# Optimization experiments

Measured on AMD Instinct MI355X. Metric: run time of the kernel, lower is better.

## Reference

```python
import jax, jax.numpy as jnp
import numpy as np

C_S = 1024
H = 16
M = 1  # num_vector_messages
B, S = 2, 1024
SQRT3 = 3.0 ** 0.5
LN_EPS = 1e-5


def setup_inputs() -> dict:
    key = jax.random.key(0)
    ks = jax.random.split(key, 8)
    s = jax.random.normal(ks[0], (B, S, C_S), dtype=jnp.float32)
    # random proper-ish frames: orthonormalize random 3x3 via QR
    A = jax.random.normal(ks[1], (B, S, 3, 3), dtype=jnp.float32)
    rot, _ = jnp.linalg.qr(A)
    trans = jax.random.normal(ks[2], (B, S, 3), dtype=jnp.float32)
    affine_mask = jnp.ones((B, S), dtype=bool)
    sequence_id = jax.random.randint(ks[3], (B, S), 0, 4, dtype=jnp.int32)
    chain_id = jax.random.randint(ks[4], (B, S), 0, 4, dtype=jnp.int32)
    dim_proj = 4 * H * 3 + H * 3 * M
    ln_w = jnp.ones((C_S,), dtype=jnp.float32)
    w_proj = jax.random.normal(ks[5], (dim_proj, C_S), dtype=jnp.float32) / np.sqrt(C_S)
    w_out = jax.random.normal(ks[6], (C_S, H * 3 * M), dtype=jnp.float32) / np.sqrt(H * 3 * M)
    dist_scale = jnp.zeros((H,), dtype=jnp.float32)
    rot_scale = jnp.zeros((H,), dtype=jnp.float32)
    return {"s": s, "rot": rot, "trans": trans, "ln_w": ln_w, "w_proj": w_proj,
            "w_out": w_out, "dist_scale": dist_scale, "rot_scale": rot_scale,
            "affine_mask": affine_mask, "sequence_id": sequence_id, "chain_id": chain_id}


def reference(s, rot, trans, ln_w, w_proj, w_out, dist_scale, rot_scale,
              affine_mask, sequence_id, chain_id):
    b, n, c = s.shape
    h, m = H, M
    NEG = jnp.finfo(s.dtype).min
    # attention bias: 1.0 for same-sequence pairs, -inf for invalid frames / cross-chain
    seq_eq = (sequence_id[:, :, None] == sequence_id[:, None, :]).astype(s.dtype)
    bias = seq_eq[:, None]  # [b,1,s,s]
    bias = jnp.where(affine_mask[:, None, None, :], bias, NEG)
    chain_diff = chain_id[:, :, None] != chain_id[:, None, :]
    bias = jnp.where(chain_diff[:, None], NEG, bias)
    # LayerNorm (no bias)
    mu = jnp.mean(s, axis=-1, keepdims=True)
    var = jnp.var(s, axis=-1, keepdims=True)
    ns = (s - mu) / jnp.sqrt(var + LN_EPS) * ln_w
    p = jnp.einsum('bsc,dc->bsd', ns, w_proj)
    n_rot = h * 2 * 3 + h * 3 * m
    vec_rot = p[..., :n_rot].reshape(b, n, 2 * h + h * m, 3)
    vec_dist = p[..., n_rot:].reshape(b, n, 2 * h, 3)
    # rotate into global frame; dist vectors also translated
    rot_vecs = jnp.einsum('bsij,bshj->bshi', rot, vec_rot)
    q_rot, k_rot, value = rot_vecs[:, :, :h], rot_vecs[:, :, h:2 * h], rot_vecs[:, :, 2 * h:]
    dist_vecs = jnp.einsum('bsij,bshj->bshi', rot, vec_dist) + trans[:, :, None, :]
    q_dist, k_dist = dist_vecs[:, :, :h], dist_vecs[:, :, h:]
    # distance term [b,h,q,k]
    qd = q_dist.transpose(0, 2, 1, 3)  # b h s 3
    kd = k_dist.transpose(0, 2, 1, 3)
    diff = qd[:, :, :, None, :] - kd[:, :, None, :, :]
    distance_term = jnp.sqrt(jnp.sum(diff * diff, axis=-1)) / SQRT3
    rotation_term = jnp.einsum('bqhd,bkhd->bhqk', q_rot, k_rot) / SQRT3
    dw = jax.nn.softplus(dist_scale)[None, :, None, None]
    rw = jax.nn.softplus(rot_scale)[None, :, None, None]
    attn = rotation_term * rw - distance_term * dw + bias
    attn = jax.nn.softmax(attn, axis=-1)
    # value: b s (h m) 3 -> b h s (m 3)
    v = value.reshape(b, n, h, m, 3).transpose(0, 2, 1, 3, 4).reshape(b, h, n, m * 3)
    out = jnp.einsum('bhqk,bhkd->bhqd', attn, v)
    out = out.reshape(b, h, n, m, 3).transpose(0, 2, 1, 3, 4).reshape(b, n, h * m, 3)
    out = jnp.einsum('bsji,bshj->bshi', rot, out)  # inverse rotation R^T
    out = out.reshape(b, n, h * m * 3)
    out = jnp.where(affine_mask[..., None], out, 0.0)
    return jnp.einsum('bsd,cd->bsc', out, w_out)
```

## Files before the change

### kernel.cpp

```cpp
#include <hip/hip_runtime.h>
#include <math.h>

#define NB 2
#define NS 1024
#define NC 1024
#define NH 16
#define DIMP 240
#define KSPLIT 16
#define AKH 16

constexpr float INV_SQRT3 = 0.57735026919f;

__global__ __launch_bounds__(256) void pre_kernel(const float* __restrict__ s,
                                                  const float* __restrict__ lnw,
                                                  float* __restrict__ ns,
                                                  const float* __restrict__ wp,
                                                  float* __restrict__ wt) {
    __shared__ float sh[64 * 61];
    int tid = threadIdx.x;
    if (blockIdx.x < NB * NS) {
        int row = blockIdx.x;
        const float4* sp = (const float4*)(s + (size_t)row * NC);
        float4 v = sp[tid];
        float sum = v.x + v.y + v.z + v.w;
        float sq  = v.x*v.x + v.y*v.y + v.z*v.z + v.w*v.w;
        #pragma unroll
        for (int off = 32; off; off >>= 1) {
            sum += __shfl_down(sum, off);
            sq  += __shfl_down(sq, off);
        }
        float* s1 = sh; float* s2 = sh + 4;
        int wave = tid >> 6;
        if ((tid & 63) == 0) { s1[wave] = sum; s2[wave] = sq; }
        __syncthreads();
        float tot   = s1[0] + s1[1] + s1[2] + s1[3];
        float totsq = s2[0] + s2[1] + s2[2] + s2[3];
        float mu  = tot * (1.0f / NC);
        float var = totsq * (1.0f / NC) - mu * mu;
        float rstd = rsqrtf(var + 1e-5f);
        float4 w = ((const float4*)lnw)[tid];
        float4 o;
        o.x = (v.x - mu) * rstd * w.x;
        o.y = (v.y - mu) * rstd * w.y;
        o.z = (v.z - mu) * rstd * w.z;
        o.w = (v.w - mu) * rstd * w.w;
        ((float4*)(ns + (size_t)row * NC))[tid] = o;
    } else {
        int bx = blockIdx.x - NB * NS;
        int k0 = (bx & 15) * 64;
        int d0 = (bx >> 4) * 60;
        float (*T)[61] = (float (*)[61])sh;
        #pragma unroll
        for (int i = 0; i < 15; i++) {
            int idx = i * 256 + tid;
            int dd = idx >> 6, kk = idx & 63;
            T[kk][dd] = wp[(size_t)(d0 + dd) * NC + k0 + kk];
        }
        __syncthreads();
        #pragma unroll
        for (int i = 0; i < 15; i++) {
            int idx = i * 256 + tid;
            int kk = idx / 60, dd = idx % 60;
            wt[(size_t)(k0 + kk) * DIMP + d0 + dd] = T[kk][dd];
        }
    }
}

__global__ __launch_bounds__(256) void proj_kernel(const float* __restrict__ ns,
                                                   const float* __restrict__ wt,
                                                   float* __restrict__ pp,
                                                   int use_atomic) {
    int tid = threadIdx.x;
    int wave = tid >> 6, lane = tid & 63;
    int row0 = blockIdx.x * 32;
    int ky = blockIdx.y;
    int k0 = ky * 64;

    __shared__ float A[32][64];
    #pragma unroll
    for (int i = 0; i < 2; i++) {
        int idx = tid + i * 256;
        int r = idx >> 4, c4 = idx & 15;
        *(float4*)&A[r][c4 * 4] = *(const float4*)(ns + (size_t)(row0 + r) * NC + k0 + c4 * 4);
    }
    __syncthreads();

    int wr0 = wave * 8;
    int c0 = lane * 4;
    bool active = c0 < DIMP;
    int c0m = active ? c0 : (DIMP - 4);
    const float* wb = wt + (size_t)k0 * DIMP + c0m;

    float acc[8][4];
    #pragma unroll
    for (int r = 0; r < 8; r++)
        #pragma unroll
        for (int c = 0; c < 4; c++) acc[r][c] = 0.0f;

    float4 wa[4], wx[4];
    #pragma unroll
    for (int j = 0; j < 4; j++) wa[j] = *(const float4*)(wb + (size_t)j * DIMP);

    for (int g = 0; g < 16; g += 2) {
        #pragma unroll
        for (int j = 0; j < 4; j++)
            wx[j] = *(const float4*)(wb + (size_t)((g + 1) * 4 + j) * DIMP);
        #pragma unroll
        for (int r = 0; r < 8; r++) {
            float4 a4 = *(const float4*)&A[wr0 + r][g * 4];
            #pragma unroll
            for (int c = 0; c < 4; c++) {
                float* ac = &acc[r][c];
                *ac = fmaf(a4.x, ((const float*)&wa[0])[c], *ac);
                *ac = fmaf(a4.y, ((const float*)&wa[1])[c], *ac);
                *ac = fmaf(a4.z, ((const float*)&wa[2])[c], *ac);
                *ac = fmaf(a4.w, ((const float*)&wa[3])[c], *ac);
            }
        }
        int kn2 = (g + 2 < 16) ? (g + 2) * 4 : 0;
        #pragma unroll
        for (int j = 0; j < 4; j++)
            wa[j] = *(const float4*)(wb + (size_t)(kn2 + j) * DIMP);
        #pragma unroll
        for (int r = 0; r < 8; r++) {
            float4 a4 = *(const float4*)&A[wr0 + r][(g + 1) * 4];
            #pragma unroll
            for (int c = 0; c < 4; c++) {
                float* ac = &acc[r][c];
                *ac = fmaf(a4.x, ((const float*)&wx[0])[c], *ac);
                *ac = fmaf(a4.y, ((const float*)&wx[1])[c], *ac);
                *ac = fmaf(a4.z, ((const float*)&wx[2])[c], *ac);
                *ac = fmaf(a4.w, ((const float*)&wx[3])[c], *ac);
            }
        }
    }
    if (active) {
        if (use_atomic) {
            #pragma unroll
            for (int r = 0; r < 8; r++)
                #pragma unroll
                for (int c = 0; c < 4; c++)
                    atomicAdd(&pp[(size_t)(row0 + wr0 + r) * DIMP + c0 + c], acc[r][c]);
        } else {
            float* dst = pp + (size_t)ky * (NB * NS * DIMP);
            #pragma unroll
            for (int r = 0; r < 8; r++)
                *(float4*)(dst + (size_t)(row0 + wr0 + r) * DIMP + c0) =
                    make_float4(acc[r][0], acc[r][1], acc[r][2], acc[r][3]);
        }
    }
}

__global__ __launch_bounds__(256) void build_kernel(const float* __restrict__ pp, int nred,
                                                    const float* __restrict__ rot,
                                                    const float* __restrict__ trans,
                                                    const float* __restrict__ dist_scale,
                                                    const float* __restrict__ rot_scale,
                                                    const int* __restrict__ seq,
                                                    const int* __restrict__ chain,
                                                    const int* __restrict__ amask,
                                                    float4* __restrict__ qrb,
                                                    float4* __restrict__ qdb,
                                                    float4* __restrict__ kp) {
    int gid = blockIdx.x * 256 + threadIdx.x;
    if (gid >= NB * NS * 80) return;
    int j  = gid % 80;
    int bs = gid / 80;
    int b  = bs >> 10;
    int si = bs & 1023;
    int off = (j < 48) ? 3 * j : 144 + 3 * (j - 48);
    float vx = 0.0f, vy = 0.0f, vz = 0.0f;
    for (int ky = 0; ky < nred; ky++) {
        const float* pr = pp + (size_t)ky * (NB * NS * DIMP) + (size_t)bs * DIMP + off;
        vx += pr[0]; vy += pr[1]; vz += pr[2];
    }
    const float* R = rot + (size_t)bs * 9;
    float ox = R[0] * vx + R[1] * vy + R[2] * vz;
    float oy = R[3] * vx + R[4] * vy + R[5] * vz;
    float oz = R[6] * vx + R[7] * vy + R[8] * vz;
    if (j >= 48) {
        ox += trans[(size_t)bs * 3 + 0];
        oy += trans[(size_t)bs * 3 + 1];
        oz += trans[(size_t)bs * 3 + 2];
    }
    if (j < 16) {
        float sc = log1pf(__expf(rot_scale[j])) * INV_SQRT3;
        qrb[(size_t)(b * NH + j) * NS + si] = make_float4(ox * sc, oy * sc, oz * sc, 0.0f);
    } else if (j < 32) {
        int h = j - 16;
        float ck = (float)chain[bs] + 1000.0f * (float)(1 - amask[bs]);
        kp[((size_t)(b * NH + h) * NS + si) * 3 + 0] = make_float4(ox, oy, oz, ck);
    } else if (j < 48) {
        int h = j - 32;
        kp[((size_t)(b * NH + h) * NS + si) * 3 + 2] = make_float4(ox, oy, oz, 0.0f);
    } else if (j < 64) {
        int h = j - 48;
        float sc = log1pf(__expf(dist_scale[h])) * INV_SQRT3;
        qdb[(size_t)(b * NH + h) * NS + si] = make_float4(ox * sc, oy * sc, oz * sc, 0.0f);
    } else {
        int h = j - 64;
        float sc = log1pf(__expf(dist_scale[h])) * INV_SQRT3;
        kp[((size_t)(b * NH + h) * NS + si) * 3 + 1] =
            make_float4(ox * sc, oy * sc, oz * sc, (float)seq[bs]);
    }
}

__global__ __launch_bounds__(256) void attn_kernel(
    const float4* __restrict__ qrb, const float4* __restrict__ qdb,
    const float4* __restrict__ kp,
    float4* __restrict__ pacc) {
    __shared__ float4 kS[192];
    int bx = blockIdx.x;
    int ks = bx & (AKH - 1), qc = (bx >> 4) & 3, bh = bx >> 6;
    int tid = threadIdx.x;
    int q = qc * 256 + tid;
    int base = bh * NS;
    const float4* kb = kp + (size_t)base * 3;

    if (tid < 192) kS[tid] = kb[(size_t)ks * 192 + tid];
    __syncthreads();

    float4 a = qrb[base + q];
    float4 d = qdb[base + q];
    float cq = kb[(size_t)q * 3 + 0].w;
    float sq = kb[(size_t)q * 3 + 1].w;

    float l = 0.0f, ax = 0.0f, ay = 0.0f, az = 0.0f;
    #pragma unroll 4
    for (int j = 0; j < 64; j++) {
        float4 f0 = kS[j * 3 + 0];
        float4 f1 = kS[j * 3 + 1];
        float4 f2 = kS[j * 3 + 2];
        float rt = fmaf(a.x, f0.x, fmaf(a.y, f0.y, a.z * f0.z));
        float dx = d.x - f1.x, dy = d.y - f1.y, dz = d.z - f1.z;
        float dist = sqrtf(fmaf(dx, dx, fmaf(dy, dy, dz * dz)));
        float dc = f0.w - cq;
        float arg = fmaf(-100.0f, fabsf(dc), rt - dist) +
                    ((f1.w == sq) ? -15.0f : -16.0f);
        float pw = __expf(arg);
        l += pw;
        ax = fmaf(pw, f2.x, ax);
        ay = fmaf(pw, f2.y, ay);
        az = fmaf(pw, f2.z, az);
    }
    pacc[(size_t)ks * (32 * NS) + base + q] = make_float4(ax, ay, az, l);
}

__global__ __launch_bounds__(256) void attnfin_kernel(const float4* __restrict__ pacc,
                                                      const float4* __restrict__ kp,
                                                      const float* __restrict__ rot,
                                                      float* __restrict__ small) {
    int i = blockIdx.x * 256 + threadIdx.x;
    int bh = i >> 10, q = i & 1023;
    int b = bh >> 4, h = bh & 15;
    float4 s = make_float4(0.0f, 0.0f, 0.0f, 0.0f);
    #pragma unroll
    for (int j = 0; j < AKH; j++) {
        float4 t = pacc[(size_t)j * (32 * NS) + i];
        s.x += t.x; s.y += t.y; s.z += t.z; s.w += t.w;
    }
    float inv = 1.0f / s.w;
    float ox = s.x * inv, oy = s.y * inv, oz = s.z * inv;
    const float* R = rot + (size_t)(b * NS + q) * 9;
    float wx = R[0] * ox + R[3] * oy + R[6] * oz;
    float wy = R[1] * ox + R[4] * oy + R[7] * oz;
    float wz = R[2] * ox + R[5] * oy + R[8] * oz;
    float cq = kp[((size_t)bh * NS + q) * 3 + 0].w;
    if (cq >= 500.0f) { wx = 0; wy = 0; wz = 0; }
    float* o = small + (size_t)(b * NS + q) * 48 + h * 3;
    o[0] = wx; o[1] = wy; o[2] = wz;
}

__global__ __launch_bounds__(256) void outgemm_kernel(const float* __restrict__ small,
                                                      const float* __restrict__ wout,
                                                      float* __restrict__ out) {
    int c  = blockIdx.y * 256 + threadIdx.x;
    int r0 = blockIdx.x * 16;
    __shared__ float sm[16][48];
    for (int i = threadIdx.x; i < 16 * 48; i += 256)
        sm[i / 48][i % 48] = small[(size_t)(r0 + i / 48) * 48 + i % 48];
    __syncthreads();
    float w[48];
    #pragma unroll
    for (int d = 0; d < 48; d += 4) {
        float4 t = *(const float4*)(wout + (size_t)c * 48 + d);
        w[d] = t.x; w[d + 1] = t.y; w[d + 2] = t.z; w[d + 3] = t.w;
    }
    #pragma unroll 4
    for (int r = 0; r < 16; r++) {
        float acc = 0.0f;
        #pragma unroll
        for (int d = 0; d < 48; d++) acc = fmaf(w[d], sm[r][d], acc);
        out[(size_t)(r0 + r) * NC + c] = acc;
    }
}

extern "C" void kernel_launch(void* const* d_in, const int* in_sizes, int n_in,
                              void* d_out, int out_size, void* d_ws, size_t ws_size,
                              hipStream_t stream) {
    const float* s     = (const float*)d_in[0];
    const float* rot   = (const float*)d_in[1];
    const float* trans = (const float*)d_in[2];
    const float* lnw   = (const float*)d_in[3];
    const float* wproj = (const float*)d_in[4];
    const float* wout  = (const float*)d_in[5];
    const float* dsc   = (const float*)d_in[6];
    const float* rsc   = (const float*)d_in[7];
    const int* amask   = (const int*)d_in[8];
    const int* seq     = (const int*)d_in[9];
    const int* chain   = (const int*)d_in[10];
    float* out = (float*)d_out;

    float* ns = (float*)d_ws;
    float4* qrb = (float4*)(ns + (size_t)NB * NS * NC);
    float4* qdb = qrb + (size_t)NB * NH * NS;
    float4* kpk = qdb + (size_t)NB * NH * NS;
    float* small = (float*)(kpk + (size_t)3 * NB * NH * NS);
    float* pp = small + (size_t)NB * NS * 48;
    float* wt = (float*)qrb;
    float4* pacc = (float4*)pp;

    size_t need = ((char*)(pp + (size_t)KSPLIT * NB * NS * DIMP)) - (char*)d_ws;
    int use_atomic = (ws_size < need) ? 1 : 0;

    pre_kernel<<<NB * NS + 64, 256, 0, stream>>>(s, lnw, ns, wproj, wt);
    if (use_atomic) {
        hipMemsetAsync(pp, 0, (size_t)NB * NS * DIMP * sizeof(float), stream);
        proj_kernel<<<dim3(64, KSPLIT), 256, 0, stream>>>(ns, wt, pp, 1);
        build_kernel<<<(NB * NS * 80 + 255) / 256, 256, 0, stream>>>(pp, 1, rot, trans, dsc, rsc,
                                                                     seq, chain, amask, qrb, qdb, kpk);
    } else {
        proj_kernel<<<dim3(64, KSPLIT), 256, 0, stream>>>(ns, wt, pp, 0);
        build_kernel<<<(NB * NS * 80 + 255) / 256, 256, 0, stream>>>(pp, KSPLIT, rot, trans, dsc, rsc,
                                                                     seq, chain, amask, qrb, qdb, kpk);
    }
    attn_kernel<<<NB * NH * 4 * AKH, 256, 0, stream>>>(qrb, qdb, kpk, pacc);
    attnfin_kernel<<<NB * NH * NS / 256, 256, 0, stream>>>(pacc, kpk, rot, small);
    outgemm_kernel<<<dim3(NB * NS / 16, 4), 256, 0, stream>>>(small, wout, out);
}
```

Baseline: 153.0 us.

## Stage projection weights in LDS and pack query chain/seq ids into query buffers

The projection GEMM now stages the 64x240 weight slice in shared memory (60KB) and streams the normalized activation rows from global memory, reversing which operand is cached. Separately, the chain and sequence ids are packed into the w lanes of the query rotation and distance buffers. This lets the attention and finalize kernels read them from the already-loaded query values instead of making extra strided loads from the key buffer. The larger shared allocation may reduce occupancy, and activation rows are now read directly from global per wave.

```diff
diff --git a/kernel.cpp b/kernel.cpp
--- a/kernel.cpp
+++ b/kernel.cpp
@@ -70,18 +70,19 @@
                                                    const float* __restrict__ wt,
                                                    float* __restrict__ pp,
                                                    int use_atomic) {
+    __shared__ float W[64 * DIMP];
     int tid = threadIdx.x;
     int wave = tid >> 6, lane = tid & 63;
     int row0 = blockIdx.x * 32;
     int ky = blockIdx.y;
     int k0 = ky * 64;
 
-    __shared__ float A[32][64];
-    #pragma unroll
-    for (int i = 0; i < 2; i++) {
-        int idx = tid + i * 256;
-        int r = idx >> 4, c4 = idx & 15;
-        *(float4*)&A[r][c4 * 4] = *(const float4*)(ns + (size_t)(row0 + r) * NC + k0 + c4 * 4);
+    {
+        const float4* src = (const float4*)(wt + (size_t)k0 * DIMP);
+        float4* dst = (float4*)W;
+        #pragma unroll
+        for (int i = 0; i < 15; i++)
+            dst[tid + i * 256] = src[tid + i * 256];
     }
     __syncthreads();
 
@@ -89,7 +90,7 @@
     int c0 = lane * 4;
     bool active = c0 < DIMP;
     int c0m = active ? c0 : (DIMP - 4);
-    const float* wb = wt + (size_t)k0 * DIMP + c0m;
+    const float* nb = ns + (size_t)(row0 + wr0) * NC + k0;
 
     float acc[8][4];
     #pragma unroll
@@ -97,40 +98,22 @@
         #pragma unroll
         for (int c = 0; c < 4; c++) acc[r][c] = 0.0f;
 
-    float4 wa[4], wx[4];
-    #pragma unroll
-    for (int j = 0; j < 4; j++) wa[j] = *(const float4*)(wb + (size_t)j * DIMP);
-
-    for (int g = 0; g < 16; g += 2) {
+    #pragma unroll 2
+    for (int g = 0; g < 16; g++) {
+        float4 w4[4];
         #pragma unroll
         for (int j = 0; j < 4; j++)
-            wx[j] = *(const float4*)(wb + (size_t)((g + 1) * 4 + j) * DIMP);
+            w4[j] = *(const float4*)&W[(g * 4 + j) * DIMP + c0m];
         #pragma unroll
         for (int r = 0; r < 8; r++) {
-            float4 a4 = *(const float4*)&A[wr0 + r][g * 4];
+            float4 a4 = *(const float4*)(nb + (size_t)r * NC + g * 4);
             #pragma unroll
             for (int c = 0; c < 4; c++) {
                 float* ac = &acc[r][c];
-                *ac = fmaf(a4.x, ((const float*)&wa[0])[c], *ac);
-                *ac = fmaf(a4.y, ((const float*)&wa[1])[c], *ac);
-                *ac = fmaf(a4.z, ((const float*)&wa[2])[c], *ac);
-                *ac = fmaf(a4.w, ((const float*)&wa[3])[c], *ac);
-            }
-        }
-        int kn2 = (g + 2 < 16) ? (g + 2) * 4 : 0;
-        #pragma unroll
-        for (int j = 0; j < 4; j++)
-            wa[j] = *(const float4*)(wb + (size_t)(kn2 + j) * DIMP);
-        #pragma unroll
-        for (int r = 0; r < 8; r++) {
-            float4 a4 = *(const float4*)&A[wr0 + r][(g + 1) * 4];
-            #pragma unroll
-            for (int c = 0; c < 4; c++) {
-                float* ac = &acc[r][c];
-                *ac = fmaf(a4.x, ((const float*)&wx[0])[c], *ac);
-                *ac = fmaf(a4.y, ((const float*)&wx[1])[c], *ac);
-                *ac = fmaf(a4.z, ((const float*)&wx[2])[c], *ac);
-                *ac = fmaf(a4.w, ((const float*)&wx[3])[c], *ac);
+                *ac = fmaf(a4.x, ((const float*)&w4[0])[c], *ac);
+                *ac = fmaf(a4.y, ((const float*)&w4[1])[c], *ac);
+                *ac = fmaf(a4.z, ((const float*)&w4[2])[c], *ac);
+                *ac = fmaf(a4.w, ((const float*)&w4[3])[c], *ac);
             }
         }
     }
@@ -185,7 +168,8 @@
     }
     if (j < 16) {
         float sc = log1pf(__expf(rot_scale[j])) * INV_SQRT3;
-        qrb[(size_t)(b * NH + j) * NS + si] = make_float4(ox * sc, oy * sc, oz * sc, 0.0f);
+        float ck = (float)chain[bs] + 1000.0f * (float)(1 - amask[bs]);
+        qrb[(size_t)(b * NH + j) * NS + si] = make_float4(ox * sc, oy * sc, oz * sc, ck);
     } else if (j < 32) {
         int h = j - 16;
         float ck = (float)chain[bs] + 1000.0f * (float)(1 - amask[bs]);
@@ -196,7 +180,8 @@
     } else if (j < 64) {
         int h = j - 48;
         float sc = log1pf(__expf(dist_scale[h])) * INV_SQRT3;
-        qdb[(size_t)(b * NH + h) * NS + si] = make_float4(ox * sc, oy * sc, oz * sc, 0.0f);
+        qdb[(size_t)(b * NH + h) * NS + si] =
+            make_float4(ox * sc, oy * sc, oz * sc, (float)seq[bs]);
     } else {
         int h = j - 64;
         float sc = log1pf(__expf(dist_scale[h])) * INV_SQRT3;
@@ -222,8 +207,7 @@
 
     float4 a = qrb[base + q];
     float4 d = qdb[base + q];
-    float cq = kb[(size_t)q * 3 + 0].w;
-    float sq = kb[(size_t)q * 3 + 1].w;
+    float cq = a.w, sq = d.w;
 
     float l = 0.0f, ax = 0.0f, ay = 0.0f, az = 0.0f;
     #pragma unroll 4
@@ -247,7 +231,7 @@
 }
 
 __global__ __launch_bounds__(256) void attnfin_kernel(const float4* __restrict__ pacc,
-                                                      const float4* __restrict__ kp,
+                                                      const float4* __restrict__ qrb,
                                                       const float* __restrict__ rot,
                                                       float* __restrict__ small) {
     int i = blockIdx.x * 256 + threadIdx.x;
@@ -265,7 +249,7 @@
     float wx = R[0] * ox + R[3] * oy + R[6] * oz;
     float wy = R[1] * ox + R[4] * oy + R[7] * oz;
     float wz = R[2] * ox + R[5] * oy + R[8] * oz;
-    float cq = kp[((size_t)bh * NS + q) * 3 + 0].w;
+    float cq = qrb[i].w;
     if (cq >= 500.0f) { wx = 0; wy = 0; wz = 0; }
     float* o = small + (size_t)(b * NS + q) * 48 + h * 3;
     o[0] = wx; o[1] = wy; o[2] = wz;
@@ -335,6 +319,6 @@
                                                                      seq, chain, amask, qrb, qdb, kpk);
     }
     attn_kernel<<<NB * NH * 4 * AKH, 256, 0, stream>>>(qrb, qdb, kpk, pacc);
-    attnfin_kernel<<<NB * NH * NS / 256, 256, 0, stream>>>(pacc, kpk, rot, small);
+    attnfin_kernel<<<NB * NH * NS / 256, 256, 0, stream>>>(pacc, qrb, rot, small);
     outgemm_kernel<<<dim3(NB * NS / 16, 4), 256, 0, stream>>>(small, wout, out);
 }
```

New measurement: 158.1 us. 3.3% more time.
